# Kernel optimization log

Hardware: AMD Instinct MI355X
Metric: run time of the kernel (lower is better)

Reference implementation:

```python
import jax, jax.numpy as jnp
import numpy as np
import math

C = 512
NUM_HEADS = 4
GROUPS = 32  # group_count(512, 32)
EPS = 1e-5


def group_norm(x, gamma, beta):
    # x: [b, c, h, w]; normalize over (c//GROUPS, h, w) per group
    b, c, h, w = x.shape
    xg = x.reshape(b, GROUPS, -1)
    mu = jnp.mean(xg, axis=-1, keepdims=True)
    var = jnp.var(xg, axis=-1, keepdims=True)
    xn = ((xg - mu) * jax.lax.rsqrt(var + EPS)).reshape(b, c, h, w)
    return xn * gamma[None, :, None, None] + beta[None, :, None, None]


def setup_inputs() -> dict:
    key = jax.random.key(0)
    ks = jax.random.split(key, 5)
    b, h, w = 2, 64, 64
    x = jax.random.normal(ks[0], (b, C, h, w), dtype=jnp.float32)
    gn_w = jnp.ones((C,), dtype=jnp.float32)
    gn_b = jnp.zeros((C,), dtype=jnp.float32)
    s_qkv = 1.0 / math.sqrt(C)
    w_qkv = jax.random.uniform(ks[1], (3 * C, C), jnp.float32, -s_qkv, s_qkv)
    b_qkv = jax.random.uniform(ks[2], (3 * C,), jnp.float32, -s_qkv, s_qkv)
    w_proj = jax.random.uniform(ks[3], (C, C), jnp.float32, -s_qkv, s_qkv)
    b_proj = jax.random.uniform(ks[4], (C,), jnp.float32, -s_qkv, s_qkv)
    return {"x": x, "gn_w": gn_w, "gn_b": gn_b, "w_qkv": w_qkv,
            "b_qkv": b_qkv, "w_proj": w_proj, "b_proj": b_proj}


def reference(x, gn_w, gn_b, w_qkv, b_qkv, w_proj, b_proj):
    b, c, h, w = x.shape
    L = h * w
    nh = NUM_HEADS
    hd = c // nh
    residual = x
    xn = group_norm(x, gn_w, gn_b).reshape(b, c, L)
    # Conv1d with kernel_size=1 == channelwise linear: [b, 3c, L]
    qkv = jnp.einsum('bcl,oc->bol', xn, w_qkv) + b_qkv[None, :, None]
    q, k, v = jnp.split(qkv, 3, axis=1)
    q = q.reshape(b, nh, hd, L)
    k = k.reshape(b, nh, hd, L)
    v = v.reshape(b, nh, hd, L)
    scores = jnp.einsum('bncd,bnce->bnde', q, k) / math.sqrt(hd)
    attn = jax.nn.softmax(scores, axis=-1)
    out = jnp.einsum('bnde,bnce->bncd', attn, v).reshape(b, c, L)
    out = jnp.einsum('bcl,oc->bol', out, w_proj) + b_proj[None, :, None]
    return out.reshape(b, c, h, w) + residual
```

## Files before the change

kernel.cpp:

```cpp
#include <hip/hip_runtime.h>
#include <math.h>

typedef __bf16 bf16;
typedef __bf16 bf16x8 __attribute__((ext_vector_type(8)));
typedef __bf16 bf16x4 __attribute__((ext_vector_type(4)));
typedef float f32x4 __attribute__((ext_vector_type(4)));

#define QSCALE (0.08838834764831845f * 1.4426950408889634f)

__device__ __forceinline__ void gll16(const bf16* g, bf16* l) {
    __builtin_amdgcn_global_load_lds((const __attribute__((address_space(1))) void*)g,
                                     (__attribute__((address_space(3))) void*)l, 16, 0, 0);
}

__global__ void k_pre(const float* __restrict__ wqkv, const float* __restrict__ wproj,
                      const float* __restrict__ x,
                      bf16* __restrict__ wqkv_b, bf16* __restrict__ wproj_b,
                      float* __restrict__ part) {
    int blk = blockIdx.x;
    if (blk < 1024) {
        int i = blk * 256 + threadIdx.x;
        const int n1 = (1536 * 512) / 4;
        float4 v;
        bf16* dst;
        if (i < n1) { v = ((const float4*)wqkv)[i];      dst = wqkv_b + (size_t)i * 4; }
        else        { v = ((const float4*)wproj)[i - n1]; dst = wproj_b + (size_t)(i - n1) * 4; }
        bf16x4 o;
        o[0] = (bf16)v.x; o[1] = (bf16)v.y; o[2] = (bf16)v.z; o[3] = (bf16)v.w;
        *(bf16x4*)dst = o;
        return;
    }
    int b2 = blk - 1024;
    int grp = b2 >> 2, p = b2 & 3;
    const float4* src = (const float4*)(x + (size_t)grp * 65536 + (size_t)p * 16384);
    float s = 0.f, ss = 0.f;
    for (int it = 0; it < 16; ++it) {
        float4 v = src[threadIdx.x + it * 256];
        s  += v.x + v.y + v.z + v.w;
        ss += v.x * v.x + v.y * v.y + v.z * v.z + v.w * v.w;
    }
    for (int off = 32; off; off >>= 1) { s += __shfl_down(s, off); ss += __shfl_down(ss, off); }
    __shared__ float rs[4], rss[4];
    int wave = threadIdx.x >> 6;
    if ((threadIdx.x & 63) == 0) { rs[wave] = s; rss[wave] = ss; }
    __syncthreads();
    if (threadIdx.x == 0) {
        part[(grp * 4 + p) * 2]     = rs[0] + rs[1] + rs[2] + rs[3];
        part[(grp * 4 + p) * 2 + 1] = rss[0] + rss[1] + rss[2] + rss[3];
    }
}

__global__ __launch_bounds__(256) void k_gn_norm_t(const float* __restrict__ x, const float* __restrict__ gw,
                                                   const float* __restrict__ gb, const float* __restrict__ part,
                                                   bf16* __restrict__ xn_t) {
    __shared__ float sX[64 * 69];
    __shared__ float sMean[4], sRstd[4];
    int b = blockIdx.z, c0 = blockIdx.y * 64, l0 = blockIdx.x * 64;
    int t = threadIdx.x;
    if (t < 4) {
        int g = b * 32 + (c0 >> 4) + t;
        float S = 0.f, SS = 0.f;
        for (int p = 0; p < 4; ++p) { S += part[(g * 4 + p) * 2]; SS += part[(g * 4 + p) * 2 + 1]; }
        float mean = S * (1.f / 65536.f);
        float var  = SS * (1.f / 65536.f) - mean * mean;
        sMean[t] = mean;
        sRstd[t] = rsqrtf(var + 1e-5f);
    }
    __syncthreads();
    int cr = t >> 4, lq = t & 15;
    const float* xp = x + ((size_t)(b * 512 + c0)) * 4096 + l0;
    for (int i = 0; i < 4; ++i) {
        int c = cr + i * 16;
        int cg = c0 + c;
        float mean = sMean[c >> 4], rstd = sRstd[c >> 4];
        float ga = gw[cg] * rstd;
        float be = gb[cg] - mean * ga;
        float4 v = *(const float4*)(xp + (size_t)c * 4096 + lq * 4);
        float* d = &sX[c * 69 + lq * 4];
        d[0] = v.x * ga + be; d[1] = v.y * ga + be; d[2] = v.z * ga + be; d[3] = v.w * ga + be;
    }
    __syncthreads();
    int lr = t >> 3, cp = t & 7;
    bf16* dst = xn_t + ((size_t)b * 4096 + l0) * 512 + c0;
    for (int i = 0; i < 2; ++i) {
        int l = lr + i * 32;
        bf16x8 o;
        for (int j = 0; j < 8; ++j) o[j] = (bf16)sX[(cp * 8 + j) * 69 + l];
        *(bf16x8*)(dst + (size_t)l * 512 + cp * 8) = o;
    }
}

__global__ __launch_bounds__(256, 3) void k_gemm_qkv(
    const bf16* __restrict__ A, const bf16* __restrict__ W, const float* __restrict__ bias,
    bf16* __restrict__ qkT, bf16* __restrict__ vb) {
    constexpr int BUF = (64 + 128) * 64;
    __shared__ bf16 smem[2 * BUF];
    int bz = blockIdx.z;
    int m0 = blockIdx.y * 64, n0 = blockIdx.x * 128;
    int tid = threadIdx.x, lane = tid & 63, wave = tid >> 6;
    int lo = lane & 15, quad = lane >> 4;
    int lr = lane >> 3, ls = lane & 7;
    int mw = (wave >> 1) * 32, nw = (wave & 1) * 64;
    const bf16* aptr[2]; int adst[2];
    for (int i = 0; i < 2; ++i) {
        int r0 = wave * 16 + i * 8;
        int row = r0 + lr;
        aptr[i] = A + (size_t)bz * (4096 * 512) + (size_t)(m0 + row) * 512 + ((ls ^ (row & 7)) * 8);
        adst[i] = r0 * 64;
    }
    const bf16* bptr[4]; int bdst[4];
    for (int i = 0; i < 4; ++i) {
        int r0 = wave * 32 + i * 8;
        int row = r0 + lr;
        bptr[i] = W + (size_t)(n0 + row) * 512 + ((ls ^ (row & 7)) * 8);
        bdst[i] = 64 * 64 + r0 * 64;
    }
    f32x4 acc[2][4] = {};
    for (int i = 0; i < 2; ++i) { gll16(aptr[i], &smem[adst[i]]); aptr[i] += 64; }
    for (int i = 0; i < 4; ++i) { gll16(bptr[i], &smem[bdst[i]]); bptr[i] += 64; }
    for (int step = 0; step < 8; ++step) {
        int cur = step & 1;
        __syncthreads();
        if (step < 7) {
            bf16* nb = &smem[(cur ^ 1) * BUF];
            for (int i = 0; i < 2; ++i) { gll16(aptr[i], nb + adst[i]); aptr[i] += 64; }
            for (int i = 0; i < 4; ++i) { gll16(bptr[i], nb + bdst[i]); bptr[i] += 64; }
        }
        const bf16* sA = &smem[cur * BUF];
        const bf16* sB = sA + 64 * 64;
        for (int kk = 0; kk < 2; ++kk) {
            bf16x8 af[2], bfr[4];
            int sw = ((kk * 4 + quad) ^ (lo & 7)) * 8;
            for (int t = 0; t < 2; ++t) af[t]  = *(const bf16x8*)&sA[(mw + t * 16 + lo) * 64 + sw];
            for (int t = 0; t < 4; ++t) bfr[t] = *(const bf16x8*)&sB[(nw + t * 16 + lo) * 64 + sw];
            for (int mt = 0; mt < 2; ++mt)
                for (int nt = 0; nt < 4; ++nt)
                    acc[mt][nt] = __builtin_amdgcn_mfma_f32_16x16x32_bf16(af[mt], bfr[nt], acc[mt][nt], 0, 0, 0);
        }
    }
    __syncthreads();
    bf16* sT = smem;
    bool isv = (n0 >= 1024);
    float sc = (n0 < 512) ? QSCALE : 1.f;
    for (int mt = 0; mt < 2; ++mt)
        for (int nt = 0; nt < 4; ++nt) {
            int c = nw + nt * 16 + lo;
            float bv = bias[n0 + c];
            for (int r = 0; r < 4; ++r) {
                int l = mw + mt * 16 + quad * 4 + r;
                float v = (acc[mt][nt][r] + bv) * sc;
                if (isv) sT[c * 72 + l]  = (bf16)v;
                else     sT[l * 136 + c] = (bf16)v;
            }
        }
    __syncthreads();
    if (isv) {
        bf16* dst = vb + (size_t)bz * (512 * 4096) + (size_t)(n0 - 1024) * 4096 + m0;
        int c = tid >> 1, h = tid & 1;
        for (int j = 0; j < 4; ++j) {
            int ch = h + j * 2;
            bf16x8 v = *(const bf16x8*)&sT[c * 72 + ch * 8];
            *(bf16x8*)(dst + (size_t)c * 4096 + ch * 8) = v;
        }
    } else {
        bf16* dst = qkT + (size_t)bz * (4096 * 1024) + (size_t)m0 * 1024 + n0;
        int l = tid >> 2, h = tid & 3;
        for (int j = 0; j < 4; ++j) {
            int ch = h + j * 4;
            bf16x8 v = *(const bf16x8*)&sT[l * 136 + ch * 8];
            *(bf16x8*)(dst + (size_t)l * 1024 + ch * 8) = v;
        }
    }
}

__global__ __launch_bounds__(256, 3) void k_gemm_proj(
    const bf16* __restrict__ W, const bf16* __restrict__ Bm,
    const float* __restrict__ bias_m,
    float* __restrict__ outf, const float* __restrict__ resid) {
    constexpr int BUF = (64 + 128) * 64;
    __shared__ bf16 smem[2 * BUF];
    int bz = blockIdx.z;
    int m0 = blockIdx.y * 64, n0 = blockIdx.x * 128;
    int tid = threadIdx.x, lane = tid & 63, wave = tid >> 6;
    int lo = lane & 15, quad = lane >> 4;
    int lr = lane >> 3, ls = lane & 7;
    int mw = (wave >> 1) * 32, nw = (wave & 1) * 64;
    const bf16* aptr[2]; int adst[2];
    for (int i = 0; i < 2; ++i) {
        int r0 = wave * 16 + i * 8;
        int row = r0 + lr;
        aptr[i] = W + (size_t)(m0 + row) * 512 + ((ls ^ (row & 7)) * 8);
        adst[i] = r0 * 64;
    }
    const bf16* bptr[4]; int bdst[4];
    for (int i = 0; i < 4; ++i) {
        int r0 = wave * 32 + i * 8;
        int row = r0 + lr;
        bptr[i] = Bm + (size_t)bz * (4096 * 512) + (size_t)(n0 + row) * 512 + ((ls ^ (row & 7)) * 8);
        bdst[i] = 64 * 64 + r0 * 64;
    }
    f32x4 acc[2][4] = {};
    for (int i = 0; i < 2; ++i) { gll16(aptr[i], &smem[adst[i]]); aptr[i] += 64; }
    for (int i = 0; i < 4; ++i) { gll16(bptr[i], &smem[bdst[i]]); bptr[i] += 64; }
    for (int step = 0; step < 8; ++step) {
        int cur = step & 1;
        __syncthreads();
        if (step < 7) {
            bf16* nb = &smem[(cur ^ 1) * BUF];
            for (int i = 0; i < 2; ++i) { gll16(aptr[i], nb + adst[i]); aptr[i] += 64; }
            for (int i = 0; i < 4; ++i) { gll16(bptr[i], nb + bdst[i]); bptr[i] += 64; }
        }
        const bf16* sA = &smem[cur * BUF];
        const bf16* sB = sA + 64 * 64;
        for (int kk = 0; kk < 2; ++kk) {
            bf16x8 af[2], bfr[4];
            int sw = ((kk * 4 + quad) ^ (lo & 7)) * 8;
            for (int t = 0; t < 2; ++t) af[t]  = *(const bf16x8*)&sA[(mw + t * 16 + lo) * 64 + sw];
            for (int t = 0; t < 4; ++t) bfr[t] = *(const bf16x8*)&sB[(nw + t * 16 + lo) * 64 + sw];
            for (int mt = 0; mt < 2; ++mt)
                for (int nt = 0; nt < 4; ++nt)
                    acc[mt][nt] = __builtin_amdgcn_mfma_f32_16x16x32_bf16(af[mt], bfr[nt], acc[mt][nt], 0, 0, 0);
        }
    }
    for (int mt = 0; mt < 2; ++mt) {
        int rowb = m0 + mw + mt * 16 + quad * 4;
        for (int nt = 0; nt < 4; ++nt) {
            int col = n0 + nw + nt * 16 + lo;
            for (int r = 0; r < 4; ++r) {
                int row = rowb + r;
                size_t idx = (size_t)bz * (512 * 4096) + (size_t)row * 4096 + col;
                outf[idx] = acc[mt][nt][r] + bias_m[row] + resid[idx];
            }
        }
    }
}

__global__ __launch_bounds__(512, 2) void k_attn(const bf16* __restrict__ qkT, const bf16* __restrict__ vmat,
                                                 bf16* __restrict__ attnT) {
    __shared__ __align__(16) char smem[104448];
    bf16* sE = (bf16*)smem;
    float* sStat = (float*)(smem + 102400);
    int bidx = blockIdx.x;
    int bh = bidx & 7;
    int bb = bh >> 2, h = bh & 3;
    int l0 = (bidx >> 3) * 128;
    int tid = threadIdx.x, lane = tid & 63, wave = tid >> 6;
    int lo = lane & 15, quad = lane >> 4;
    int a = wave & 3, b2 = wave >> 2;
    int lr16 = lane >> 4, ls16 = lane & 15;
    int lr8 = lane >> 3, ls8 = lane & 7;
    const bf16* qbase = qkT + ((size_t)bb * 4096 + l0) * 1024 + h * 128;
    const bf16* kbase = qkT + (size_t)bb * 4096 * 1024 + 512 + h * 128;
    const bf16* vbase = vmat + (size_t)(bb * 512 + h * 128) * 4096;
    for (int i = 0; i < 4; ++i) {
        int r0 = wave * 16 + i * 4;
        int row = r0 + lr16;
        gll16(qbase + (size_t)row * 1024 + ((ls16 ^ (row & 15)) * 8), sE + r0 * 128);
    }
    __syncthreads();
    bf16x8 qf[2][4];
    for (int nt = 0; nt < 2; ++nt) {
        int row = a * 32 + nt * 16 + lo;
        for (int kk = 0; kk < 4; ++kk)
            qf[nt][kk] = *(const bf16x8*)&sE[row * 128 + (((kk * 4 + quad) ^ lo) * 8)];
    }
    __syncthreads();
    const bf16* kptr[2]; int kdst[2];
    const bf16* vptr[2]; int vdst[2];
    for (int i = 0; i < 2; ++i) {
        int r0 = wave * 8 + i * 4;
        int row = r0 + lr16;
        kptr[i] = kbase + (size_t)row * 1024 + ((ls16 ^ (row & 15)) * 8);
        kdst[i] = r0 * 128;
        int s0 = wave * 16 + i * 8;
        int srow = s0 + lr8;
        vptr[i] = vbase + (size_t)srow * 4096 + ((ls8 ^ (srow & 7)) * 8);
        vdst[i] = s0 * 64;
    }
    bf16* sPe = (bf16*)(smem + 65536) + wave * 1280;
    float l_r[2];
    l_r[0] = l_r[1] = 0.f;
    f32x4 oacc[8][2] = {};
    for (int i = 0; i < 2; ++i) { gll16(kptr[i], sE + kdst[i]); kptr[i] += (size_t)64 * 1024; }
    for (int i = 0; i < 2; ++i) { gll16(vptr[i], sE + 16384 + vdst[i]); vptr[i] += 64; }
    for (int it = 0; it < 64; ++it) {
        int cur = it & 1;
        __syncthreads();
        if (it < 63) {
            bf16* nk = sE + (cur ^ 1) * 8192;
            bf16* nv = sE + 16384 + (cur ^ 1) * 8192;
            for (int i = 0; i < 2; ++i) { gll16(kptr[i], nk + kdst[i]); kptr[i] += (size_t)64 * 1024; }
            for (int i = 0; i < 2; ++i) { gll16(vptr[i], nv + vdst[i]); vptr[i] += 64; }
        }
        const bf16* sK = sE + cur * 8192;
        const bf16* sV = sE + 16384 + cur * 8192;
        f32x4 s[2][2];
        for (int mt = 0; mt < 2; ++mt) {
            int krow = b2 * 32 + mt * 16 + lo;
            bf16x8 kf[4];
            for (int kk = 0; kk < 4; ++kk)
                kf[kk] = *(const bf16x8*)&sK[krow * 128 + (((kk * 4 + quad) ^ lo) * 8)];
            for (int nt = 0; nt < 2; ++nt) {
                f32x4 acc = {};
                for (int kk = 0; kk < 4; ++kk)
                    acc = __builtin_amdgcn_mfma_f32_16x16x32_bf16(kf[kk], qf[nt][kk], acc, 0, 0, 0);
                s[mt][nt] = acc;
            }
        }
        for (int nt = 0; nt < 2; ++nt) {
            float sm = 0.f;
            for (int mt = 0; mt < 2; ++mt) {
                bf16x4 pk;
                for (int r = 0; r < 4; ++r) {
                    float pv = __builtin_amdgcn_exp2f(s[mt][nt][r]);
                    sm += pv;
                    pk[r] = (bf16)pv;
                }
                *(bf16x4*)&sPe[(nt * 16 + lo) * 40 + mt * 16 + quad * 4] = pk;
            }
            l_r[nt] += sm;
        }
        bf16x8 pf[2];
        for (int nt = 0; nt < 2; ++nt)
            pf[nt] = *(const bf16x8*)&sPe[(nt * 16 + lo) * 40 + quad * 8];
        for (int mt2 = 0; mt2 < 8; ++mt2) {
            bf16x8 vf = *(const bf16x8*)&sV[(mt2 * 16 + lo) * 64 + (((b2 * 4 + quad) ^ (lo & 7)) * 8)];
            for (int nt = 0; nt < 2; ++nt)
                oacc[mt2][nt] = __builtin_amdgcn_mfma_f32_16x16x32_bf16(vf, pf[nt], oacc[mt2][nt], 0, 0, 0);
        }
    }
    for (int nt = 0; nt < 2; ++nt) {
        l_r[nt] += __shfl_xor(l_r[nt], 16);
        l_r[nt] += __shfl_xor(l_r[nt], 32);
    }
    __syncthreads();
    if (quad == 0) {
        for (int nt = 0; nt < 2; ++nt) {
            int qb = a * 32 + nt * 16 + lo;
            sStat[qb * 2 + b2] = l_r[nt];
        }
    }
    __syncthreads();
    float inv[2];
    for (int nt = 0; nt < 2; ++nt) {
        int qb = a * 32 + nt * 16 + lo;
        inv[nt] = 1.f / (sStat[qb * 2] + sStat[qb * 2 + 1]);
    }
    float* sOm = (float*)smem;
    bf16* sOut = (bf16*)(smem + 67584);
    if (b2 == 1) {
        for (int mt2 = 0; mt2 < 8; ++mt2)
            for (int nt = 0; nt < 2; ++nt)
                for (int r = 0; r < 4; ++r) {
                    int vc = mt2 * 16 + quad * 4 + r;
                    sOm[a * 4224 + vc * 33 + nt * 16 + lo] = oacc[mt2][nt][r];
                }
    }
    __syncthreads();
    if (b2 == 0) {
        for (int mt2 = 0; mt2 < 8; ++mt2)
            for (int nt = 0; nt < 2; ++nt)
                for (int r = 0; r < 4; ++r) {
                    int vc = mt2 * 16 + quad * 4 + r;
                    float v = (oacc[mt2][nt][r] + sOm[a * 4224 + vc * 33 + nt * 16 + lo]) * inv[nt];
                    sOut[(a * 32 + nt * 16 + lo) * 136 + vc] = (bf16)v;
                }
    }
    __syncthreads();
    bf16* dst = attnT + ((size_t)bb * 4096 + l0) * 512 + h * 128;
    for (int i = 0; i < 4; ++i) {
        int row = (tid >> 4) + i * 32;
        int chunk = tid & 15;
        bf16x8 v = *(const bf16x8*)&sOut[row * 136 + chunk * 8];
        *(bf16x8*)(dst + (size_t)row * 512 + chunk * 8) = v;
    }
}

extern "C" void kernel_launch(void* const* d_in, const int* in_sizes, int n_in,
                              void* d_out, int out_size, void* d_ws, size_t ws_size,
                              hipStream_t stream) {
    const float* x      = (const float*)d_in[0];
    const float* gn_w   = (const float*)d_in[1];
    const float* gn_b   = (const float*)d_in[2];
    const float* w_qkv  = (const float*)d_in[3];
    const float* b_qkv  = (const float*)d_in[4];
    const float* w_proj = (const float*)d_in[5];
    const float* b_proj = (const float*)d_in[6];
    float* out = (float*)d_out;
    char* ws = (char*)d_ws;
    bf16* wqkv_b  = (bf16*)(ws + 0);
    bf16* wproj_b = (bf16*)(ws + 1572864);
    bf16* xn_t    = (bf16*)(ws + 2097152);
    bf16* qkT     = (bf16*)(ws + 10485760);
    bf16* vb      = (bf16*)(ws + 27262976);
    bf16* attnT   = (bf16*)(ws + 35651584);
    float* part   = (float*)(ws + 44040192);

    k_pre<<<1280, 256, 0, stream>>>(w_qkv, w_proj, x, wqkv_b, wproj_b, part);
    k_gn_norm_t<<<dim3(64, 8, 2), 256, 0, stream>>>(x, gn_w, gn_b, part, xn_t);
    k_gemm_qkv<<<dim3(12, 64, 2), 256, 0, stream>>>(xn_t, wqkv_b, b_qkv, qkT, vb);
    k_attn<<<256, 512, 0, stream>>>(qkT, vb, attnT);
    k_gemm_proj<<<dim3(32, 8, 2), 256, 0, stream>>>(wproj_b, attnT, b_proj, out, x);
}
```

Before: 188.3 us.

## Split attention block into 16 waves with 16 queries each and MFMA priority

```diff
diff --git a/kernel.cpp b/kernel.cpp
--- a/kernel.cpp
+++ b/kernel.cpp
@@ -235,141 +235,121 @@
     }
 }
 
-__global__ __launch_bounds__(512, 2) void k_attn(const bf16* __restrict__ qkT, const bf16* __restrict__ vmat,
-                                                 bf16* __restrict__ attnT) {
+__global__ __launch_bounds__(1024, 4) void k_attn(const bf16* __restrict__ qkT, const bf16* __restrict__ vmat,
+                                                  bf16* __restrict__ attnT) {
     __shared__ __align__(16) char smem[104448];
     bf16* sE = (bf16*)smem;
-    float* sStat = (float*)(smem + 102400);
+    float* sStat = (float*)(smem + 86016);
     int bidx = blockIdx.x;
     int bh = bidx & 7;
     int bb = bh >> 2, h = bh & 3;
     int l0 = (bidx >> 3) * 128;
     int tid = threadIdx.x, lane = tid & 63, wave = tid >> 6;
     int lo = lane & 15, quad = lane >> 4;
-    int a = wave & 3, b2 = wave >> 2;
+    int a = wave & 7, b2 = wave >> 3;
     int lr16 = lane >> 4, ls16 = lane & 15;
     int lr8 = lane >> 3, ls8 = lane & 7;
     const bf16* qbase = qkT + ((size_t)bb * 4096 + l0) * 1024 + h * 128;
     const bf16* kbase = qkT + (size_t)bb * 4096 * 1024 + 512 + h * 128;
     const bf16* vbase = vmat + (size_t)(bb * 512 + h * 128) * 4096;
-    for (int i = 0; i < 4; ++i) {
-        int r0 = wave * 16 + i * 4;
+    for (int i = 0; i < 2; ++i) {
+        int r0 = wave * 8 + i * 4;
         int row = r0 + lr16;
         gll16(qbase + (size_t)row * 1024 + ((ls16 ^ (row & 15)) * 8), sE + r0 * 128);
     }
     __syncthreads();
-    bf16x8 qf[2][4];
-    for (int nt = 0; nt < 2; ++nt) {
-        int row = a * 32 + nt * 16 + lo;
+    bf16x8 qf[4];
+    {
+        int row = a * 16 + lo;
         for (int kk = 0; kk < 4; ++kk)
-            qf[nt][kk] = *(const bf16x8*)&sE[row * 128 + (((kk * 4 + quad) ^ lo) * 8)];
-    }
-    __syncthreads();
-    const bf16* kptr[2]; int kdst[2];
-    const bf16* vptr[2]; int vdst[2];
-    for (int i = 0; i < 2; ++i) {
-        int r0 = wave * 8 + i * 4;
-        int row = r0 + lr16;
-        kptr[i] = kbase + (size_t)row * 1024 + ((ls16 ^ (row & 15)) * 8);
-        kdst[i] = r0 * 128;
-        int s0 = wave * 16 + i * 8;
-        int srow = s0 + lr8;
-        vptr[i] = vbase + (size_t)srow * 4096 + ((ls8 ^ (srow & 7)) * 8);
-        vdst[i] = s0 * 64;
-    }
-    bf16* sPe = (bf16*)(smem + 65536) + wave * 1280;
-    float l_r[2];
-    l_r[0] = l_r[1] = 0.f;
-    f32x4 oacc[8][2] = {};
-    for (int i = 0; i < 2; ++i) { gll16(kptr[i], sE + kdst[i]); kptr[i] += (size_t)64 * 1024; }
-    for (int i = 0; i < 2; ++i) { gll16(vptr[i], sE + 16384 + vdst[i]); vptr[i] += 64; }
+            qf[kk] = *(const bf16x8*)&sE[row * 128 + (((kk * 4 + quad) ^ lo) * 8)];
+    }
+    __syncthreads();
+    const bf16* kptr; int kdst;
+    const bf16* vptr; int vdst;
+    {
+        int row = wave * 4 + lr16;
+        kptr = kbase + (size_t)row * 1024 + ((ls16 ^ (row & 15)) * 8);
+        kdst = wave * 4 * 128;
+        int srow = wave * 8 + lr8;
+        vptr = vbase + (size_t)srow * 4096 + ((ls8 ^ (srow & 7)) * 8);
+        vdst = wave * 8 * 64;
+    }
+    bf16* sPe = (bf16*)(smem + 65536) + wave * 640;
+    float l_r = 0.f;
+    f32x4 oacc[8] = {};
+    gll16(kptr, sE + kdst); kptr += (size_t)64 * 1024;
+    gll16(vptr, sE + 16384 + vdst); vptr += 64;
     for (int it = 0; it < 64; ++it) {
         int cur = it & 1;
         __syncthreads();
         if (it < 63) {
             bf16* nk = sE + (cur ^ 1) * 8192;
             bf16* nv = sE + 16384 + (cur ^ 1) * 8192;
-            for (int i = 0; i < 2; ++i) { gll16(kptr[i], nk + kdst[i]); kptr[i] += (size_t)64 * 1024; }
-            for (int i = 0; i < 2; ++i) { gll16(vptr[i], nv + vdst[i]); vptr[i] += 64; }
+            gll16(kptr, nk + kdst); kptr += (size_t)64 * 1024;
+            gll16(vptr, nv + vdst); vptr += 64;
         }
         const bf16* sK = sE + cur * 8192;
         const bf16* sV = sE + 16384 + cur * 8192;
-        f32x4 s[2][2];
+        f32x4 s[2];
+        __builtin_amdgcn_s_setprio(1);
         for (int mt = 0; mt < 2; ++mt) {
             int krow = b2 * 32 + mt * 16 + lo;
             bf16x8 kf[4];
             for (int kk = 0; kk < 4; ++kk)
                 kf[kk] = *(const bf16x8*)&sK[krow * 128 + (((kk * 4 + quad) ^ lo) * 8)];
-            for (int nt = 0; nt < 2; ++nt) {
-                f32x4 acc = {};
-                for (int kk = 0; kk < 4; ++kk)
-                    acc = __builtin_amdgcn_mfma_f32_16x16x32_bf16(kf[kk], qf[nt][kk], acc, 0, 0, 0);
-                s[mt][nt] = acc;
-            }
-        }
-        for (int nt = 0; nt < 2; ++nt) {
-            float sm = 0.f;
-            for (int mt = 0; mt < 2; ++mt) {
-                bf16x4 pk;
-                for (int r = 0; r < 4; ++r) {
-                    float pv = __builtin_amdgcn_exp2f(s[mt][nt][r]);
-                    sm += pv;
-                    pk[r] = (bf16)pv;
-                }
-                *(bf16x4*)&sPe[(nt * 16 + lo) * 40 + mt * 16 + quad * 4] = pk;
-            }
-            l_r[nt] += sm;
-        }
-        bf16x8 pf[2];
-        for (int nt = 0; nt < 2; ++nt)
-            pf[nt] = *(const bf16x8*)&sPe[(nt * 16 + lo) * 40 + quad * 8];
+            f32x4 acc = {};
+            for (int kk = 0; kk < 4; ++kk)
+                acc = __builtin_amdgcn_mfma_f32_16x16x32_bf16(kf[kk], qf[kk], acc, 0, 0, 0);
+            s[mt] = acc;
+        }
+        __builtin_amdgcn_s_setprio(0);
+        float sm = 0.f;
+        for (int mt = 0; mt < 2; ++mt) {
+            bf16x4 pk;
+            for (int r = 0; r < 4; ++r) {
+                float pv = __builtin_amdgcn_exp2f(s[mt][r]);
+                sm += pv;
+                pk[r] = (bf16)pv;
+            }
+            *(bf16x4*)&sPe[lo * 40 + mt * 16 + quad * 4] = pk;
+        }
+        l_r += sm;
+        bf16x8 pf = *(const bf16x8*)&sPe[lo * 40 + quad * 8];
+        __builtin_amdgcn_s_setprio(1);
         for (int mt2 = 0; mt2 < 8; ++mt2) {
             bf16x8 vf = *(const bf16x8*)&sV[(mt2 * 16 + lo) * 64 + (((b2 * 4 + quad) ^ (lo & 7)) * 8)];
-            for (int nt = 0; nt < 2; ++nt)
-                oacc[mt2][nt] = __builtin_amdgcn_mfma_f32_16x16x32_bf16(vf, pf[nt], oacc[mt2][nt], 0, 0, 0);
-        }
-    }
-    for (int nt = 0; nt < 2; ++nt) {
-        l_r[nt] += __shfl_xor(l_r[nt], 16);
-        l_r[nt] += __shfl_xor(l_r[nt], 32);
-    }
-    __syncthreads();
-    if (quad == 0) {
-        for (int nt = 0; nt < 2; ++nt) {
-            int qb = a * 32 + nt * 16 + lo;
-            sStat[qb * 2 + b2] = l_r[nt];
-        }
-    }
-    __syncthreads();
-    float inv[2];
-    for (int nt = 0; nt < 2; ++nt) {
-        int qb = a * 32 + nt * 16 + lo;
-        inv[nt] = 1.f / (sStat[qb * 2] + sStat[qb * 2 + 1]);
-    }
+            oacc[mt2] = __builtin_amdgcn_mfma_f32_16x16x32_bf16(vf, pf, oacc[mt2], 0, 0, 0);
+        }
+        __builtin_amdgcn_s_setprio(0);
+    }
+    l_r += __shfl_xor(l_r, 16);
+    l_r += __shfl_xor(l_r, 32);
+    if (quad == 0) sStat[(a * 16 + lo) * 2 + b2] = l_r;
+    __syncthreads();
+    float inv = 1.f / (sStat[(a * 16 + lo) * 2] + sStat[(a * 16 + lo) * 2 + 1]);
     float* sOm = (float*)smem;
-    bf16* sOut = (bf16*)(smem + 67584);
+    bf16* sOut = (bf16*)(smem + 69632);
     if (b2 == 1) {
         for (int mt2 = 0; mt2 < 8; ++mt2)
-            for (int nt = 0; nt < 2; ++nt)
-                for (int r = 0; r < 4; ++r) {
-                    int vc = mt2 * 16 + quad * 4 + r;
-                    sOm[a * 4224 + vc * 33 + nt * 16 + lo] = oacc[mt2][nt][r];
-                }
+            for (int r = 0; r < 4; ++r) {
+                int vc = mt2 * 16 + quad * 4 + r;
+                sOm[a * 2176 + vc * 17 + lo] = oacc[mt2][r];
+            }
     }
     __syncthreads();
     if (b2 == 0) {
         for (int mt2 = 0; mt2 < 8; ++mt2)
-            for (int nt = 0; nt < 2; ++nt)
-                for (int r = 0; r < 4; ++r) {
-                    int vc = mt2 * 16 + quad * 4 + r;
-                    float v = (oacc[mt2][nt][r] + sOm[a * 4224 + vc * 33 + nt * 16 + lo]) * inv[nt];
-                    sOut[(a * 32 + nt * 16 + lo) * 136 + vc] = (bf16)v;
-                }
+            for (int r = 0; r < 4; ++r) {
+                int vc = mt2 * 16 + quad * 4 + r;
+                float v = (oacc[mt2][r] + sOm[a * 2176 + vc * 17 + lo]) * inv;
+                sOut[(a * 16 + lo) * 136 + vc] = (bf16)v;
+            }
     }
     __syncthreads();
     bf16* dst = attnT + ((size_t)bb * 4096 + l0) * 512 + h * 128;
-    for (int i = 0; i < 4; ++i) {
-        int row = (tid >> 4) + i * 32;
+    for (int i = 0; i < 2; ++i) {
+        int row = (tid >> 4) + i * 64;
         int chunk = tid & 15;
         bf16x8 v = *(const bf16x8*)&sOut[row * 136 + chunk * 8];
         *(bf16x8*)(dst + (size_t)row * 512 + chunk * 8) = v;
@@ -399,6 +379,6 @@
     k_pre<<<1280, 256, 0, stream>>>(w_qkv, w_proj, x, wqkv_b, wproj_b, part);
     k_gn_norm_t<<<dim3(64, 8, 2), 256, 0, stream>>>(x, gn_w, gn_b, part, xn_t);
     k_gemm_qkv<<<dim3(12, 64, 2), 256, 0, stream>>>(xn_t, wqkv_b, b_qkv, qkT, vb);
-    k_attn<<<256, 512, 0, stream>>>(qkT, vb, attnT);
+    k_attn<<<256, 1024, 0, stream>>>(qkT, vb, attnT);
     k_gemm_proj<<<dim3(32, 8, 2), 256, 0, stream>>>(wproj_b, attnT, b_proj, out, x);
 }
```

After: 189.2 us. No clear change (+0.5%).

## Software-pipeline attention loop so QK^T of next tile overlaps softmax and PV

Applied to the files above, without the earlier changes.

```diff
diff --git a/kernel.cpp b/kernel.cpp
--- a/kernel.cpp
+++ b/kernel.cpp
@@ -281,20 +281,40 @@
     float l_r[2];
     l_r[0] = l_r[1] = 0.f;
     f32x4 oacc[8][2] = {};
+    f32x4 sp[2][2];
     for (int i = 0; i < 2; ++i) { gll16(kptr[i], sE + kdst[i]); kptr[i] += (size_t)64 * 1024; }
+    __syncthreads();
+    for (int i = 0; i < 2; ++i) { gll16(kptr[i], sE + 8192 + kdst[i]); kptr[i] += (size_t)64 * 1024; }
     for (int i = 0; i < 2; ++i) { gll16(vptr[i], sE + 16384 + vdst[i]); vptr[i] += 64; }
-    for (int it = 0; it < 64; ++it) {
+    __builtin_amdgcn_s_setprio(1);
+    for (int mt = 0; mt < 2; ++mt) {
+        int krow = b2 * 32 + mt * 16 + lo;
+        bf16x8 kf[4];
+        for (int kk = 0; kk < 4; ++kk)
+            kf[kk] = *(const bf16x8*)&sE[krow * 128 + (((kk * 4 + quad) ^ lo) * 8)];
+        for (int nt = 0; nt < 2; ++nt) {
+            f32x4 acc = {};
+            for (int kk = 0; kk < 4; ++kk)
+                acc = __builtin_amdgcn_mfma_f32_16x16x32_bf16(kf[kk], qf[nt][kk], acc, 0, 0, 0);
+            sp[mt][nt] = acc;
+        }
+    }
+    __builtin_amdgcn_s_setprio(0);
+    for (int it = 1; it < 64; ++it) {
         int cur = it & 1;
         __syncthreads();
         if (it < 63) {
             bf16* nk = sE + (cur ^ 1) * 8192;
-            bf16* nv = sE + 16384 + (cur ^ 1) * 8192;
             for (int i = 0; i < 2; ++i) { gll16(kptr[i], nk + kdst[i]); kptr[i] += (size_t)64 * 1024; }
+        }
+        {
+            bf16* nv = sE + 16384 + cur * 8192;
             for (int i = 0; i < 2; ++i) { gll16(vptr[i], nv + vdst[i]); vptr[i] += 64; }
         }
-        const bf16* sK = sE + cur * 8192;
-        const bf16* sV = sE + 16384 + cur * 8192;
-        f32x4 s[2][2];
+        const bf16* sK  = sE + cur * 8192;
+        const bf16* sVp = sE + 16384 + (cur ^ 1) * 8192;
+        f32x4 sc[2][2];
+        __builtin_amdgcn_s_setprio(1);
         for (int mt = 0; mt < 2; ++mt) {
             int krow = b2 * 32 + mt * 16 + lo;
             bf16x8 kf[4];
@@ -304,15 +324,16 @@
                 f32x4 acc = {};
                 for (int kk = 0; kk < 4; ++kk)
                     acc = __builtin_amdgcn_mfma_f32_16x16x32_bf16(kf[kk], qf[nt][kk], acc, 0, 0, 0);
-                s[mt][nt] = acc;
+                sc[mt][nt] = acc;
             }
         }
+        __builtin_amdgcn_s_setprio(0);
         for (int nt = 0; nt < 2; ++nt) {
             float sm = 0.f;
             for (int mt = 0; mt < 2; ++mt) {
                 bf16x4 pk;
                 for (int r = 0; r < 4; ++r) {
-                    float pv = __builtin_amdgcn_exp2f(s[mt][nt][r]);
+                    float pv = __builtin_amdgcn_exp2f(sp[mt][nt][r]);
                     sm += pv;
                     pk[r] = (bf16)pv;
                 }
@@ -323,8 +344,38 @@
         bf16x8 pf[2];
         for (int nt = 0; nt < 2; ++nt)
             pf[nt] = *(const bf16x8*)&sPe[(nt * 16 + lo) * 40 + quad * 8];
+        __builtin_amdgcn_s_setprio(1);
         for (int mt2 = 0; mt2 < 8; ++mt2) {
-            bf16x8 vf = *(const bf16x8*)&sV[(mt2 * 16 + lo) * 64 + (((b2 * 4 + quad) ^ (lo & 7)) * 8)];
+            bf16x8 vf = *(const bf16x8*)&sVp[(mt2 * 16 + lo) * 64 + (((b2 * 4 + quad) ^ (lo & 7)) * 8)];
+            for (int nt = 0; nt < 2; ++nt)
+                oacc[mt2][nt] = __builtin_amdgcn_mfma_f32_16x16x32_bf16(vf, pf[nt], oacc[mt2][nt], 0, 0, 0);
+        }
+        __builtin_amdgcn_s_setprio(0);
+        for (int mt = 0; mt < 2; ++mt)
+            for (int nt = 0; nt < 2; ++nt)
+                sp[mt][nt] = sc[mt][nt];
+    }
+    __syncthreads();
+    {
+        const bf16* sVp = sE + 16384 + 8192;
+        for (int nt = 0; nt < 2; ++nt) {
+            float sm = 0.f;
+            for (int mt = 0; mt < 2; ++mt) {
+                bf16x4 pk;
+                for (int r = 0; r < 4; ++r) {
+                    float pv = __builtin_amdgcn_exp2f(sp[mt][nt][r]);
+                    sm += pv;
+                    pk[r] = (bf16)pv;
+                }
+                *(bf16x4*)&sPe[(nt * 16 + lo) * 40 + mt * 16 + quad * 4] = pk;
+            }
+            l_r[nt] += sm;
+        }
+        bf16x8 pf[2];
+        for (int nt = 0; nt < 2; ++nt)
+            pf[nt] = *(const bf16x8*)&sPe[(nt * 16 + lo) * 40 + quad * 8];
+        for (int mt2 = 0; mt2 < 8; ++mt2) {
+            bf16x8 vf = *(const bf16x8*)&sVp[(mt2 * 16 + lo) * 64 + (((b2 * 4 + quad) ^ (lo & 7)) * 8)];
             for (int nt = 0; nt < 2; ++nt)
                 oacc[mt2][nt] = __builtin_amdgcn_mfma_f32_16x16x32_bf16(vf, pf[nt], oacc[mt2][nt], 0, 0, 0);
         }
@@ -333,7 +384,6 @@
         l_r[nt] += __shfl_xor(l_r[nt], 16);
         l_r[nt] += __shfl_xor(l_r[nt], 32);
     }
-    __syncthreads();
     if (quad == 0) {
         for (int nt = 0; nt < 2; ++nt) {
             int qb = a * 32 + nt * 16 + lo;
```

Measured after the change: 189.6 us. Within noise of the previous version (+0.7%).

## Load V tiles straight into registers with register double-buffering in attention loop

Applied to the files above, without the earlier changes.

```diff
diff --git a/kernel.cpp b/kernel.cpp
--- a/kernel.cpp
+++ b/kernel.cpp
@@ -237,7 +237,7 @@
 
 __global__ __launch_bounds__(512, 2) void k_attn(const bf16* __restrict__ qkT, const bf16* __restrict__ vmat,
                                                  bf16* __restrict__ attnT) {
-    __shared__ __align__(16) char smem[104448];
+    __shared__ __align__(16) char smem[103424];
     bf16* sE = (bf16*)smem;
     float* sStat = (float*)(smem + 102400);
     int bidx = blockIdx.x;
@@ -248,7 +248,6 @@
     int lo = lane & 15, quad = lane >> 4;
     int a = wave & 3, b2 = wave >> 2;
     int lr16 = lane >> 4, ls16 = lane & 15;
-    int lr8 = lane >> 3, ls8 = lane & 7;
     const bf16* qbase = qkT + ((size_t)bb * 4096 + l0) * 1024 + h * 128;
     const bf16* kbase = qkT + (size_t)bb * 4096 * 1024 + 512 + h * 128;
     const bf16* vbase = vmat + (size_t)(bb * 512 + h * 128) * 4096;
@@ -266,74 +265,79 @@
     }
     __syncthreads();
     const bf16* kptr[2]; int kdst[2];
-    const bf16* vptr[2]; int vdst[2];
     for (int i = 0; i < 2; ++i) {
         int r0 = wave * 8 + i * 4;
         int row = r0 + lr16;
         kptr[i] = kbase + (size_t)row * 1024 + ((ls16 ^ (row & 15)) * 8);
         kdst[i] = r0 * 128;
-        int s0 = wave * 16 + i * 8;
-        int srow = s0 + lr8;
-        vptr[i] = vbase + (size_t)srow * 4096 + ((ls8 ^ (srow & 7)) * 8);
-        vdst[i] = s0 * 64;
-    }
-    bf16* sPe = (bf16*)(smem + 65536) + wave * 1280;
+    }
+    const bf16* vgb = vbase + (size_t)lo * 4096 + b2 * 32 + quad * 8;
+    bf16* sPe = (bf16*)(smem + 32768) + wave * 1280;
     float l_r[2];
     l_r[0] = l_r[1] = 0.f;
     f32x4 oacc[8][2] = {};
+    bf16x8 vA[8], vB[8];
     for (int i = 0; i < 2; ++i) { gll16(kptr[i], sE + kdst[i]); kptr[i] += (size_t)64 * 1024; }
-    for (int i = 0; i < 2; ++i) { gll16(vptr[i], sE + 16384 + vdst[i]); vptr[i] += 64; }
-    for (int it = 0; it < 64; ++it) {
-        int cur = it & 1;
-        __syncthreads();
-        if (it < 63) {
-            bf16* nk = sE + (cur ^ 1) * 8192;
-            bf16* nv = sE + 16384 + (cur ^ 1) * 8192;
-            for (int i = 0; i < 2; ++i) { gll16(kptr[i], nk + kdst[i]); kptr[i] += (size_t)64 * 1024; }
-            for (int i = 0; i < 2; ++i) { gll16(vptr[i], nv + vdst[i]); vptr[i] += 64; }
-        }
-        const bf16* sK = sE + cur * 8192;
-        const bf16* sV = sE + 16384 + cur * 8192;
-        f32x4 s[2][2];
-        for (int mt = 0; mt < 2; ++mt) {
-            int krow = b2 * 32 + mt * 16 + lo;
-            bf16x8 kf[4];
-            for (int kk = 0; kk < 4; ++kk)
-                kf[kk] = *(const bf16x8*)&sK[krow * 128 + (((kk * 4 + quad) ^ lo) * 8)];
-            for (int nt = 0; nt < 2; ++nt) {
-                f32x4 acc = {};
-                for (int kk = 0; kk < 4; ++kk)
-                    acc = __builtin_amdgcn_mfma_f32_16x16x32_bf16(kf[kk], qf[nt][kk], acc, 0, 0, 0);
-                s[mt][nt] = acc;
-            }
-        }
-        for (int nt = 0; nt < 2; ++nt) {
-            float sm = 0.f;
-            for (int mt = 0; mt < 2; ++mt) {
-                bf16x4 pk;
-                for (int r = 0; r < 4; ++r) {
-                    float pv = __builtin_amdgcn_exp2f(s[mt][nt][r]);
-                    sm += pv;
-                    pk[r] = (bf16)pv;
-                }
-                *(bf16x4*)&sPe[(nt * 16 + lo) * 40 + mt * 16 + quad * 4] = pk;
-            }
-            l_r[nt] += sm;
-        }
-        bf16x8 pf[2];
-        for (int nt = 0; nt < 2; ++nt)
-            pf[nt] = *(const bf16x8*)&sPe[(nt * 16 + lo) * 40 + quad * 8];
-        for (int mt2 = 0; mt2 < 8; ++mt2) {
-            bf16x8 vf = *(const bf16x8*)&sV[(mt2 * 16 + lo) * 64 + (((b2 * 4 + quad) ^ (lo & 7)) * 8)];
-            for (int nt = 0; nt < 2; ++nt)
-                oacc[mt2][nt] = __builtin_amdgcn_mfma_f32_16x16x32_bf16(vf, pf[nt], oacc[mt2][nt], 0, 0, 0);
-        }
-    }
+    for (int m = 0; m < 8; ++m) vA[m] = *(const bf16x8*)(vgb + (size_t)m * 16 * 4096);
+
+#define ATTN_BODY(IT, VC, VN)                                                                       \
+    {                                                                                               \
+        int cur = (IT) & 1;                                                                         \
+        __syncthreads();                         \
+        if ((IT) < 63) {                                                                            \
+            bf16* nk = sE + (cur ^ 1) * 8192;                                                       \
+            for (int i = 0; i < 2; ++i) { gll16(kptr[i], nk + kdst[i]); kptr[i] += (size_t)64 * 1024; } \
+            const bf16* vp = vgb + (size_t)((IT) + 1) * 64;                                         \
+            for (int m = 0; m < 8; ++m) VN[m] = *(const bf16x8*)(vp + (size_t)m * 16 * 4096);       \
+        }                                                                                           \
+        const bf16* sK = sE + cur * 8192;                                                           \
+        f32x4 s[2][2];                                                                              \
+        __builtin_amdgcn_s_setprio(1);                                                              \
+        for (int mt = 0; mt < 2; ++mt) {                                                            \
+            int krow = b2 * 32 + mt * 16 + lo;                                                      \
+            bf16x8 kf[4];                                                                           \
+            for (int kk = 0; kk < 4; ++kk)                                                          \
+                kf[kk] = *(const bf16x8*)&sK[krow * 128 + (((kk * 4 + quad) ^ lo) * 8)];            \
+            for (int nt = 0; nt < 2; ++nt) {                                                        \
+                f32x4 acc = {};                                                                     \
+                for (int kk = 0; kk < 4; ++kk)                                                      \
+                    acc = __builtin_amdgcn_mfma_f32_16x16x32_bf16(kf[kk], qf[nt][kk], acc, 0, 0, 0);\
+                s[mt][nt] = acc;                                                                    \
+            }                                                                                       \
+        }                                                                                           \
+        __builtin_amdgcn_s_setprio(0);                                                              \
+        for (int nt = 0; nt < 2; ++nt) {                                                            \
+            float sm = 0.f;                                                                         \
+            for (int mt = 0; mt < 2; ++mt) {                                                        \
+                bf16x4 pk;                                                                          \
+                for (int r = 0; r < 4; ++r) {                                                       \
+                    float pv = __builtin_amdgcn_exp2f(s[mt][nt][r]);                                \
+                    sm += pv;                                                                       \
+                    pk[r] = (bf16)pv;                                                               \
+                }                                                                                   \
+                *(bf16x4*)&sPe[(nt * 16 + lo) * 40 + mt * 16 + quad * 4] = pk;                      \
+            }                                                                                       \
+            l_r[nt] += sm;                                                                          \
+        }                                                                                           \
+        bf16x8 pf[2];                                                                               \
+        for (int nt = 0; nt < 2; ++nt)                                                              \
+            pf[nt] = *(const bf16x8*)&sPe[(nt * 16 + lo) * 40 + quad * 8];                          \
+        __builtin_amdgcn_s_setprio(1);                                                              \
+        for (int m = 0; m < 8; ++m)                                                                 \
+            for (int nt = 0; nt < 2; ++nt)                                                          \
+                oacc[m][nt] = __builtin_amdgcn_mfma_f32_16x16x32_bf16(VC[m], pf[nt], oacc[m][nt], 0, 0, 0); \
+        __builtin_amdgcn_s_setprio(0);                                                              \
+    }
+
+    for (int it2 = 0; it2 < 64; it2 += 2) {
+        ATTN_BODY(it2, vA, vB);
+        ATTN_BODY(it2 + 1, vB, vA);
+    }
+#undef ATTN_BODY
     for (int nt = 0; nt < 2; ++nt) {
         l_r[nt] += __shfl_xor(l_r[nt], 16);
         l_r[nt] += __shfl_xor(l_r[nt], 32);
     }
-    __syncthreads();
     if (quad == 0) {
         for (int nt = 0; nt < 2; ++nt) {
             int qb = a * 32 + nt * 16 + lo;
```

Measured after the change: 263.8 us. 1.4x slower.
